# Optimization experiments

Hardware: AMD Instinct MI355X
Metric: run time of the kernel (lower is better)

The kernel has to match this reference:

```python
import jax, jax.numpy as jnp
import numpy as np
import math

N, J = 8192, 22  # N = batch*frames (per-frame calls are independent), J = num_joint


def _layernorm(x, g, b, eps=1e-5):
    m = jnp.mean(x, axis=-1, keepdims=True)
    v = jnp.var(x, axis=-1, keepdims=True)
    return (x - m) * jax.lax.rsqrt(v + eps) * g + b


def _attention(x, Wqkv, bqkv, Wo, bo, heads):
    # x: [B, n, d]; matches torch Attention (scale = d**-0.5)
    B, n, d = x.shape
    hd = d // heads
    qkv = (x @ Wqkv + bqkv).reshape(B, n, 3, heads, hd).transpose(2, 0, 3, 1, 4)
    q, k, v = qkv[0], qkv[1], qkv[2]  # [B, h, n, hd]
    dots = jnp.einsum('bhid,bhjd->bhij', q, k) * (d ** -0.5)
    attn = jax.nn.softmax(dots, axis=-1)
    out = jnp.einsum('bhij,bhjd->bhid', attn, v)
    out = out.transpose(0, 2, 1, 3).reshape(B, n, -1)
    return out @ Wo + bo


def _encoder(x, tok_W, tok_b, qkv_W, qkv_b, o_W, o_b, ln_g, ln_b, m1_W, m1_b, m2_W, m2_b, heads):
    tok = x @ tok_W + tok_b                                   # [B, J, 64]
    h = _attention(tok, qkv_W, qkv_b, o_W, o_b, heads)        # [B, J, out_dim]
    hn = _layernorm(h, ln_g, ln_b)
    mlp = jax.nn.relu(hn @ m1_W + m1_b) @ m2_W + m2_b
    return h + mlp                                            # Residual(LN+MLP)


def _sinusoidal_pe(max_len, dim):
    pos = np.arange(max_len)[:, None].astype(np.float32)
    div = np.exp(np.arange(0, dim, 2, dtype=np.float32) * (-math.log(10000.0) / dim))
    pe = np.zeros((max_len, dim), dtype=np.float32)
    pe[:, 0::2] = np.sin(pos * div)
    pe[:, 1::2] = np.cos(pos * div)
    return jnp.asarray(pe)


def setup_inputs() -> dict:
    key = jax.random.key(0)
    ks = iter(jax.random.split(key, 64))
    rn = lambda shape, s=0.1: jax.random.normal(next(ks), shape, dtype=jnp.float32) * s
    inp = {
        'q_t': jax.random.normal(next(ks), (N, J, 4), dtype=jnp.float32),
        'skelA': jax.random.normal(next(ks), (N, J, 3), dtype=jnp.float32),
        'skelB': jax.random.normal(next(ks), (N, J, 3), dtype=jnp.float32),
        'quat_mean': jax.random.normal(next(ks), (J, 4), dtype=jnp.float32) * 0.1,
        'quat_std': jax.random.uniform(next(ks), (J, 4), dtype=jnp.float32, minval=0.5, maxval=1.5),
        # QuatEncoder params
        'qe_tok_W': rn((4, 64)), 'qe_tok_b': jnp.zeros((64,), jnp.float32),
        'qe_qkv_W': rn((64, 192)), 'qe_qkv_b': jnp.zeros((192,), jnp.float32),
        'qe_o_W': rn((64, 256)), 'qe_o_b': jnp.zeros((256,), jnp.float32),
        'qe_ln_g': jnp.ones((256,), jnp.float32), 'qe_ln_b': jnp.zeros((256,), jnp.float32),
        'qe_m1_W': rn((256, 512)), 'qe_m1_b': jnp.zeros((512,), jnp.float32),
        'qe_m2_W': rn((512, 256)), 'qe_m2_b': jnp.zeros((256,), jnp.float32),
        # shared SeklEncoder params
        'se_tok_W': rn((3, 64)), 'se_tok_b': jnp.zeros((64,), jnp.float32),
        'se_qkv_W': rn((64, 192)), 'se_qkv_b': jnp.zeros((192,), jnp.float32),
        'se_o_W': rn((64, 128)), 'se_o_b': jnp.zeros((128,), jnp.float32),
        'se_ln_g': jnp.ones((128,), jnp.float32), 'se_ln_b': jnp.zeros((128,), jnp.float32),
        'se_m1_W': rn((128, 256)), 'se_m1_b': jnp.zeros((256,), jnp.float32),
        'se_m2_W': rn((256, 128)), 'se_m2_b': jnp.zeros((128,), jnp.float32),
        # head
        'emb_W': rn((512, 128)), 'emb_b': jnp.zeros((128,), jnp.float32),
        'del_W': rn((128, 4)), 'del_b': jnp.zeros((4,), jnp.float32),
    }
    return inp


def reference(q_t, skelA, skelB, quat_mean, quat_std,
              qe_tok_W, qe_tok_b, qe_qkv_W, qe_qkv_b, qe_o_W, qe_o_b,
              qe_ln_g, qe_ln_b, qe_m1_W, qe_m1_b, qe_m2_W, qe_m2_b,
              se_tok_W, se_tok_b, se_qkv_W, se_qkv_b, se_o_W, se_o_b,
              se_ln_g, se_ln_b, se_m1_W, se_m1_b, se_m2_W, se_m2_b,
              emb_W, emb_b, del_W, del_b):
    q_embed = _encoder(q_t, qe_tok_W, qe_tok_b, qe_qkv_W, qe_qkv_b, qe_o_W, qe_o_b,
                       qe_ln_g, qe_ln_b, qe_m1_W, qe_m1_b, qe_m2_W, qe_m2_b, heads=4)   # [N,J,256]
    sA = _encoder(skelA, se_tok_W, se_tok_b, se_qkv_W, se_qkv_b, se_o_W, se_o_b,
                  se_ln_g, se_ln_b, se_m1_W, se_m1_b, se_m2_W, se_m2_b, heads=2)        # [N,J,128]
    sB = _encoder(skelB, se_tok_W, se_tok_b, se_qkv_W, se_qkv_b, se_o_W, se_o_b,
                  se_ln_g, se_ln_b, se_m1_W, se_m1_b, se_m2_W, se_m2_b, heads=2)        # [N,J,128]
    cat = jnp.concatenate([q_embed, sA, sB], axis=-1)                                   # [N,J,512]
    dim = cat.shape[-1]
    pe = _sinusoidal_pe(J, dim)
    pos = cat * math.sqrt(dim) + pe[None, :, :]
    embed = jax.nn.relu(pos @ emb_W + emb_b)                                            # [N,J,128]
    delta = embed @ del_W + del_b                                                       # [N,J,4]
    delta = delta * quat_std + quat_mean
    # normalized()
    lengths = jnp.sqrt(jnp.sum(delta * delta, axis=-1, keepdims=True))
    return delta / lengths
```

## Files before the change

### kernel.cpp

```cpp
#include <hip/hip_runtime.h>
#include <hip/hip_bf16.h>
#include <math.h>

#define NJ 22
#define MROWS 44
#define PROWS 48
#define NRT 3

typedef float f4 __attribute__((ext_vector_type(4)));
typedef _Float16 h8 __attribute__((ext_vector_type(8)));

#define WOFF_QE_QKV 0
#define WOFF_QE_O   24576
#define WOFF_QE_M1  57344
#define WOFF_QE_M2  319488
#define WOFF_SE_QKV 581632
#define WOFF_SE_O   606208
#define WOFF_SE_M1  622592
#define WOFF_SE_M2  688128
#define WOFF_EMB    753664
#define W_TOTAL     884736

struct Smem {
    _Float16 XH[PROWS * 256];
    __align__(16) char U[PROWS * 128 * 4];
    float LNp[PROWS * 4], LNq[PROWS * 4];
    float Sx[MROWS * 4];
};

struct Args {
    const float *q_t, *skelA, *skelB;
    const float *qe_o_b, *qe_ln_g, *qe_ln_b, *qe_m1_b, *qe_m2_b;
    const float *se_o_b, *se_ln_g, *se_ln_b, *se_m1_b, *se_m2_b;
    const float *fqe, *fse;
    const _Float16 *W;
    _Float16 *cat;
};

__device__ __forceinline__ int swz(int r, int c) {
    return (((c >> 3) ^ (r & 7)) << 3) | (c & 7);
}

template<int NI, int KSTEPS, int LDA>
__device__ __forceinline__ void mfma_gemm(f4 (&acc)[NI][NRT],
        const _Float16 *AH,
        const _Float16 *BH, const _Float16 *BL,
        int wK, int koff, int w, int l) {
    const int m = l & 15, q = l >> 4;
#pragma unroll 1
    for (int s = 0; s < KSTEPS; s++) {
        const int ka = s * 32 + q * 8;
        h8 a[NRT];
#pragma unroll
        for (int rt = 0; rt < NRT; rt++) {
            int r = rt * 16 + m;
            a[rt] = *(const h8 *)(AH + r * LDA + (((ka >> 3) ^ (r & 7)) << 3));
        }
#pragma unroll
        for (int i = 0; i < NI; i++) {
            int n = (w + 4 * i) * 16 + m;
            int boff = n * wK + koff + ka;
            h8 bh = *(const h8 *)(BH + boff);
            h8 bl = *(const h8 *)(BL + boff);
#pragma unroll
            for (int rt = 0; rt < NRT; rt++) {
                acc[i][rt] = __builtin_amdgcn_mfma_f32_16x16x32_f16(a[rt], bh, acc[i][rt], 0, 0, 0);
                acc[i][rt] = __builtin_amdgcn_mfma_f32_16x16x32_f16(a[rt], bl, acc[i][rt], 0, 0, 0);
            }
        }
    }
}

template<int NH, int HD>
__device__ __forceinline__ void attention(Smem &sm, int t) {
    constexpr int SPL = HD / 16;
    if (t < NH * MROWS * SPL) {
        const int half = t & (SPL - 1);
        const int ur = t / SPL;
        const int hh = ur / MROWS;
        const int rr = ur - hh * MROWS;
        const int jb = (rr >= NJ) ? NJ : 0;
        const float *KF = (const float *)sm.U;
        const float *VF = KF + PROWS * 64;
        const int c0 = 64 + hh * HD + half * 16;
        float qv[16];
#pragma unroll
        for (int g = 0; g < 2; g++) {
            h8 qh = *(const h8 *)(sm.XH + rr * 256 + swz(rr, c0 + g * 8));
#pragma unroll
            for (int d = 0; d < 8; d++) qv[g * 8 + d] = (float)qh[d];
        }
        float s[NJ];
        float mx = -1e30f;
#pragma unroll
        for (int j = 0; j < NJ; j++) {
            const float *kp = KF + (jb + j) * 64 + hh * HD + half * 16;
            float acc = 0.f;
#pragma unroll
            for (int d = 0; d < 16; d += 4) {
                float4 v = *(const float4 *)(kp + d);
                acc += qv[d] * v.x + qv[d + 1] * v.y + qv[d + 2] * v.z + qv[d + 3] * v.w;
            }
            if constexpr (SPL == 2) acc += __shfl_xor(acc, 1);
            s[j] = acc * 0.125f;
            mx = fmaxf(mx, s[j]);
        }
        float sum = 0.f;
#pragma unroll
        for (int j = 0; j < NJ; j++) { s[j] = __expf(s[j] - mx); sum += s[j]; }
        float inv = 1.f / sum;
        float o[16];
#pragma unroll
        for (int d = 0; d < 16; d++) o[d] = 0.f;
#pragma unroll
        for (int j = 0; j < NJ; j++) {
            float p = s[j] * inv;
            const float *vp = VF + (jb + j) * 64 + hh * HD + half * 16;
#pragma unroll
            for (int d = 0; d < 16; d += 4) {
                float4 v = *(const float4 *)(vp + d);
                o[d] = fmaf(p, v.x, o[d]);       o[d + 1] = fmaf(p, v.y, o[d + 1]);
                o[d + 2] = fmaf(p, v.z, o[d + 2]); o[d + 3] = fmaf(p, v.w, o[d + 3]);
            }
        }
        const int cw = hh * HD + half * 16;
#pragma unroll
        for (int g = 0; g < 2; g++) {
            h8 oh;
#pragma unroll
            for (int d = 0; d < 8; d++) oh[d] = (_Float16)o[g * 8 + d];
            *(h8 *)(sm.XH + rr * 256 + swz(rr, cw + g * 8)) = oh;
        }
    }
}

template<int D, int NH, int TK>
__device__ __forceinline__ void encode(Smem &sm, const float *__restrict__ xg,
        const float *__restrict__ F,
        const float *__restrict__ oB,
        const float *__restrict__ lnG,  const float *__restrict__ lnB,
        const float *__restrict__ m1B,  const float *__restrict__ m2B,
        const _Float16 *__restrict__ Wo,
        const _Float16 *__restrict__ Wm1, const _Float16 *__restrict__ Wm2,
        _Float16 *__restrict__ catb, int catoff, int t, int w, int l) {
    constexpr int NI = D / 64;
    constexpr int HID = 2 * D;
    const int m = l & 15, q = l >> 4;
    const float *FW = F, *Fb = F + TK * 192;

    if (t < MROWS * TK) sm.Sx[t] = xg[t];
    __syncthreads();
    {
        float *KV = (float *)sm.U;
#pragma unroll
        for (int i = 0; i < 11; i++) {
            int r = w + 4 * i;
            float x0 = sm.Sx[r * TK + 0];
            float x1 = sm.Sx[r * TK + 1];
            float x2 = sm.Sx[r * TK + 2];
            float x3 = (TK == 4) ? sm.Sx[r * TK + 3] : 0.f;
#pragma unroll
            for (int kk = 0; kk < 3; kk++) {
                int c = kk * 64 + l;
                float acc = Fb[c];
                acc = fmaf(x0, FW[0 * 192 + c], acc);
                acc = fmaf(x1, FW[1 * 192 + c], acc);
                acc = fmaf(x2, FW[2 * 192 + c], acc);
                if (TK == 4) acc = fmaf(x3, FW[3 * 192 + c], acc);
                if (kk == 0)      sm.XH[r * 256 + swz(r, 64 + l)] = (_Float16)acc;
                else if (kk == 1) KV[r * 64 + l] = acc;
                else              KV[PROWS * 64 + r * 64 + l] = acc;
            }
        }
    }
    __syncthreads();
    attention<NH, 64 / NH>(sm, t);
    __syncthreads();
    f4 res[NI][NRT];
#pragma unroll
    for (int i = 0; i < NI; i++)
#pragma unroll
        for (int rt = 0; rt < NRT; rt++) res[i][rt] = (f4){0.f, 0.f, 0.f, 0.f};
    mfma_gemm<NI, 2, 256>(res, sm.XH, Wo, Wo + D * 64, 64, 0, w, l);
#pragma unroll
    for (int i = 0; i < NI; i++) {
        float b = oB[(w + 4 * i) * 16 + m];
#pragma unroll
        for (int rt = 0; rt < NRT; rt++)
#pragma unroll
            for (int e = 0; e < 4; e++) res[i][rt][e] += b;
    }
#pragma unroll
    for (int rt = 0; rt < NRT; rt++)
#pragma unroll
        for (int e = 0; e < 4; e++) {
            int r = rt * 16 + q * 4 + e;
            float s1 = 0.f, s2 = 0.f;
#pragma unroll
            for (int i = 0; i < NI; i++) {
                float v = res[i][rt][e];
                s1 += v; s2 = fmaf(v, v, s2);
            }
#pragma unroll
            for (int off = 8; off > 0; off >>= 1) {
                s1 += __shfl_xor(s1, off);
                s2 += __shfl_xor(s2, off);
            }
            if (m == 0) { sm.LNp[r * 4 + w] = s1; sm.LNq[r * 4 + w] = s2; }
        }
    __syncthreads();
    {
        float gv[NI], bv[NI];
#pragma unroll
        for (int i = 0; i < NI; i++) {
            int c = (w + 4 * i) * 16 + m;
            gv[i] = lnG[c]; bv[i] = lnB[c];
        }
#pragma unroll
        for (int rt = 0; rt < NRT; rt++)
#pragma unroll
            for (int e = 0; e < 4; e++) {
                int r = rt * 16 + q * 4 + e;
                float s1 = sm.LNp[r * 4] + sm.LNp[r * 4 + 1] + sm.LNp[r * 4 + 2] + sm.LNp[r * 4 + 3];
                float s2 = sm.LNq[r * 4] + sm.LNq[r * 4 + 1] + sm.LNq[r * 4 + 2] + sm.LNq[r * 4 + 3];
                float mean = s1 * (1.f / D);
                float var = s2 * (1.f / D) - mean * mean;
                float rinv = rsqrtf(fmaxf(var, 0.f) + 1e-5f);
#pragma unroll
                for (int i = 0; i < NI; i++) {
                    int c = (w + 4 * i) * 16 + m;
                    float v = (res[i][rt][e] - mean) * rinv * gv[i] + bv[i];
                    sm.XH[r * 256 + swz(r, c)] = (_Float16)v;
                }
            }
    }
    __syncthreads();
#pragma unroll 1
    for (int cb = 0; cb < HID / 128; cb++) {
        f4 h1[2][NRT];
#pragma unroll
        for (int i = 0; i < 2; i++)
#pragma unroll
            for (int rt = 0; rt < NRT; rt++) h1[i][rt] = (f4){0.f, 0.f, 0.f, 0.f};
        mfma_gemm<2, D / 32, 256>(h1, sm.XH,
                                  Wm1 + cb * 128 * D, Wm1 + HID * D + cb * 128 * D, D, 0, w, l);
        _Float16 *HH = (_Float16 *)sm.U + (cb & 1) * (PROWS * 128);
#pragma unroll
        for (int i = 0; i < 2; i++) {
            int c = (w + 4 * i) * 16 + m;
            float b = m1B[cb * 128 + c];
#pragma unroll
            for (int rt = 0; rt < NRT; rt++)
#pragma unroll
                for (int e = 0; e < 4; e++) {
                    int r = rt * 16 + q * 4 + e;
                    HH[r * 128 + swz(r, c)] = (_Float16)fmaxf(h1[i][rt][e] + b, 0.f);
                }
        }
        __syncthreads();
        mfma_gemm<NI, 4, 128>(res, HH, Wm2, Wm2 + D * HID, HID, cb * 128, w, l);
    }
#pragma unroll
    for (int i = 0; i < NI; i++) {
        int c = (w + 4 * i) * 16 + m;
        float b = m2B[c];
#pragma unroll
        for (int rt = 0; rt < NRT; rt++)
#pragma unroll
            for (int e = 0; e < 4; e++) {
                int r = rt * 16 + q * 4 + e;
                if (r < MROWS)
                    catb[r * 512 + catoff + c] = (_Float16)(res[i][rt][e] + b);
            }
    }
}

__global__ __launch_bounds__(256, 2) void fused_kernel(Args A) {
    __shared__ __align__(16) Smem sm;
    const int t = threadIdx.x, w = t >> 6, l = t & 63;
    const int blk = blockIdx.x;

    for (int i = t; i < 4 * 256; i += 256) {
        int r = MROWS + (i >> 8), c = i & 255;
        sm.XH[r * 256 + c] = (_Float16)0.f;
    }

    const _Float16 *W = A.W;
    _Float16 *catb = A.cat + (size_t)blk * MROWS * 512;

    encode<256, 4, 4>(sm, A.q_t + blk * MROWS * 4, A.fqe,
                      A.qe_o_b, A.qe_ln_g, A.qe_ln_b, A.qe_m1_b, A.qe_m2_b,
                      W + WOFF_QE_O, W + WOFF_QE_M1, W + WOFF_QE_M2,
                      catb, 0, t, w, l);
    encode<128, 2, 3>(sm, A.skelA + blk * MROWS * 3, A.fse,
                      A.se_o_b, A.se_ln_g, A.se_ln_b, A.se_m1_b, A.se_m2_b,
                      W + WOFF_SE_O, W + WOFF_SE_M1, W + WOFF_SE_M2,
                      catb, 256, t, w, l);
    encode<128, 2, 3>(sm, A.skelB + blk * MROWS * 3, A.fse,
                      A.se_o_b, A.se_ln_g, A.se_ln_b, A.se_m1_b, A.se_m2_b,
                      W + WOFF_SE_O, W + WOFF_SE_M1, W + WOFF_SE_M2,
                      catb, 384, t, w, l);
}

struct HeadArgs {
    const _Float16 *cat;
    const _Float16 *W;
    const float *P;
    const float *del_W, *del_b, *quat_mean, *quat_std;
    float *out;
    int R;
};

#define ELD 132

__global__ __launch_bounds__(256, 4) void head_kernel(HeadArgs A) {
    __shared__ float E[64 * ELD];
    __shared__ float Sd[64 * 4];
    const int t = threadIdx.x, w = t >> 6, l = t & 63;
    const int m = l & 15, q = l >> 4;
    const int rowbase = blockIdx.x * 64;
    const _Float16 *BH = A.W + WOFF_EMB;
    const _Float16 *BL = BH + 128 * 512;

    f4 acc[2][4];
#pragma unroll
    for (int i = 0; i < 2; i++)
#pragma unroll
        for (int rt = 0; rt < 4; rt++) acc[i][rt] = (f4){0.f, 0.f, 0.f, 0.f};

#pragma unroll 1
    for (int s = 0; s < 16; s++) {
        const int ka = s * 32 + q * 8;
        h8 a[4];
#pragma unroll
        for (int rt = 0; rt < 4; rt++) {
            int rg = rowbase + rt * 16 + m;
            rg = rg < A.R ? rg : A.R - 1;
            a[rt] = *(const h8 *)(A.cat + (size_t)rg * 512 + ka);
        }
#pragma unroll
        for (int i = 0; i < 2; i++) {
            int n = (w + 4 * i) * 16 + m;
            h8 bh = *(const h8 *)(BH + n * 512 + ka);
            h8 bl = *(const h8 *)(BL + n * 512 + ka);
#pragma unroll
            for (int rt = 0; rt < 4; rt++) {
                acc[i][rt] = __builtin_amdgcn_mfma_f32_16x16x32_f16(a[rt], bh, acc[i][rt], 0, 0, 0);
                acc[i][rt] = __builtin_amdgcn_mfma_f32_16x16x32_f16(a[rt], bl, acc[i][rt], 0, 0, 0);
            }
        }
    }
#pragma unroll
    for (int i = 0; i < 2; i++) {
        int c = (w + 4 * i) * 16 + m;
#pragma unroll
        for (int rt = 0; rt < 4; rt++)
#pragma unroll
            for (int e = 0; e < 4; e++) {
                int r = rt * 16 + q * 4 + e;
                int j = (rowbase + r) % NJ;
                float v = fmaf(22.627416997969522f, acc[i][rt][e], A.P[j * 128 + c]);
                E[r * ELD + c] = fmaxf(v, 0.f);
            }
    }
    __syncthreads();
    {
        int r = t >> 2, d = t & 3;
        float a2 = A.del_b[d];
        const float *Er = E + r * ELD;
#pragma unroll 4
        for (int c4 = 0; c4 < 32; c4++) {
            float4 ev = *(const float4 *)(Er + c4 * 4);
            a2 = fmaf(ev.x, A.del_W[(c4 * 4 + 0) * 4 + d], a2);
            a2 = fmaf(ev.y, A.del_W[(c4 * 4 + 1) * 4 + d], a2);
            a2 = fmaf(ev.z, A.del_W[(c4 * 4 + 2) * 4 + d], a2);
            a2 = fmaf(ev.w, A.del_W[(c4 * 4 + 3) * 4 + d], a2);
        }
        int j = (rowbase + r) % NJ;
        Sd[t] = fmaf(a2, A.quat_std[j * 4 + d], A.quat_mean[j * 4 + d]);
    }
    __syncthreads();
    {
        int r = t >> 2;
        int rg = rowbase + r;
        if (rg < A.R) {
            float x0 = Sd[r * 4], x1 = Sd[r * 4 + 1];
            float x2 = Sd[r * 4 + 2], x3 = Sd[r * 4 + 3];
            float inv = 1.f / sqrtf(x0 * x0 + x1 * x1 + x2 * x2 + x3 * x3);
            A.out[(size_t)rg * 4 + (t & 3)] = Sd[t] * inv;
        }
    }
}

struct WDesc { const float *W; int K; int N; int off; };
struct SplitArgs { WDesc d[9]; _Float16 *out; };

__global__ void split_kernel(SplitArgs a) {
    WDesc d = a.d[blockIdx.y];
    int e = blockIdx.x * 256 + threadIdx.x;
    int tot = d.K * d.N;
    if (e < tot) {
        int n = e / d.K, k = e - n * d.K;
        float v = d.W[k * d.N + n];
        _Float16 h = (_Float16)v;
        a.out[d.off + e] = h;
        a.out[d.off + tot + e] = (_Float16)(v - (float)h);
    }
}

struct FoldArgs {
    const float *qe_tokW, *qe_tokB, *qe_qkvW, *qe_qkvB;
    const float *se_tokW, *se_tokB, *se_qkvW, *se_qkvB;
    float *fqe, *fse;
};

__global__ void fold_kernel(FoldArgs a) {
    int c = threadIdx.x;
    if (blockIdx.x == 0) {
#pragma unroll
        for (int kk = 0; kk < 4; kk++) {
            float acc = 0.f;
            for (int k = 0; k < 64; k++)
                acc = fmaf(a.qe_tokW[kk * 64 + k], a.qe_qkvW[k * 192 + c], acc);
            a.fqe[kk * 192 + c] = acc;
        }
        float acc = a.qe_qkvB[c];
        for (int k = 0; k < 64; k++)
            acc = fmaf(a.qe_tokB[k], a.qe_qkvW[k * 192 + c], acc);
        a.fqe[4 * 192 + c] = acc;
    } else {
#pragma unroll
        for (int kk = 0; kk < 3; kk++) {
            float acc = 0.f;
            for (int k = 0; k < 64; k++)
                acc = fmaf(a.se_tokW[kk * 64 + k], a.se_qkvW[k * 192 + c], acc);
            a.fse[kk * 192 + c] = acc;
        }
        float acc = a.se_qkvB[c];
        for (int k = 0; k < 64; k++)
            acc = fmaf(a.se_tokB[k], a.se_qkvW[k * 192 + c], acc);
        a.fse[3 * 192 + c] = acc;
    }
}

__global__ void pe_emb_kernel(const float *__restrict__ emb_W,
                              const float *__restrict__ emb_b, float *P) {
    int r = blockIdx.x;
    int c = threadIdx.x;
    float acc = emb_b[c];
    const float k = -2.f * logf(10000.f) / 512.f;
    for (int i = 0; i < 256; i++) {
        float ang = (float)r * expf((float)i * k);
        acc = fmaf(sinf(ang), emb_W[(2 * i) * 128 + c], acc);
        acc = fmaf(cosf(ang), emb_W[(2 * i + 1) * 128 + c], acc);
    }
    P[r * 128 + c] = acc;
}

extern "C" void kernel_launch(void *const *d_in, const int *in_sizes, int n_in,
                              void *d_out, int out_size, void *d_ws, size_t ws_size,
                              hipStream_t stream) {
    const float **in = (const float **)d_in;
    float *dwf = (float *)d_ws;
    float *P   = dwf;
    float *FQE = dwf + 2816;
    float *FSE = dwf + 3776;
    _Float16 *W = (_Float16 *)(dwf + 4544);
    _Float16 *cat = W + W_TOTAL;

    Args A;
    A.q_t = in[0]; A.skelA = in[1]; A.skelB = in[2];
    A.qe_o_b = in[10]; A.qe_ln_g = in[11]; A.qe_ln_b = in[12];
    A.qe_m1_b = in[14]; A.qe_m2_b = in[16];
    A.se_o_b = in[22]; A.se_ln_g = in[23]; A.se_ln_b = in[24];
    A.se_m1_b = in[26]; A.se_m2_b = in[28];
    A.fqe = FQE; A.fse = FSE;
    A.W = W; A.cat = cat;

    SplitArgs sa;
    sa.d[0] = { in[7],  64, 192, WOFF_QE_QKV };
    sa.d[1] = { in[9],  64, 256, WOFF_QE_O };
    sa.d[2] = { in[13], 256, 512, WOFF_QE_M1 };
    sa.d[3] = { in[15], 512, 256, WOFF_QE_M2 };
    sa.d[4] = { in[19], 64, 192, WOFF_SE_QKV };
    sa.d[5] = { in[21], 64, 128, WOFF_SE_O };
    sa.d[6] = { in[25], 128, 256, WOFF_SE_M1 };
    sa.d[7] = { in[27], 256, 128, WOFF_SE_M2 };
    sa.d[8] = { in[29], 512, 128, WOFF_EMB };
    sa.out = W;

    FoldArgs fa;
    fa.qe_tokW = in[5];  fa.qe_tokB = in[6];  fa.qe_qkvW = in[7];  fa.qe_qkvB = in[8];
    fa.se_tokW = in[17]; fa.se_tokB = in[18]; fa.se_qkvW = in[19]; fa.se_qkvB = in[20];
    fa.fqe = FQE; fa.fse = FSE;

    int n_items = in_sizes[0] / (NJ * 4);
    int blocks = n_items / 2;
    int R = n_items * NJ;

    HeadArgs H;
    H.cat = cat; H.W = W; H.P = P;
    H.del_W = in[31]; H.del_b = in[32]; H.quat_mean = in[3]; H.quat_std = in[4];
    H.out = (float *)d_out; H.R = R;

    split_kernel<<<dim3(512, 9), 256, 0, stream>>>(sa);
    fold_kernel<<<2, 192, 0, stream>>>(fa);
    pe_emb_kernel<<<NJ, 128, 0, stream>>>(in[29], in[30], P);
    fused_kernel<<<blocks, 256, 0, stream>>>(A);
    head_kernel<<<(R + 63) / 64, 256, 0, stream>>>(H);
}
```

Before: 1.307 ms.

## Fuse embedding head into encoder kernel, keeping concatenated features in LDS

The head GEMM, ReLU, delta projection and normalization now run inside the fused encoder kernel. The encoder outputs stay in shared memory (the skeleton ones in new LDS buffers, the quaternion one in XH), so the fp16 concatenated tensor is no longer written to and re-read from global memory and one launch is dropped. Encoder order is swapped so the larger output lands last in XH. In exchange, LDS use per block grows, which may pressure occupancy. Each block also reloads the embedding weights and runs the GEMM on padded 48-row tiles.

```diff
diff --git a/kernel.cpp b/kernel.cpp
--- a/kernel.cpp
+++ b/kernel.cpp
@@ -24,6 +24,7 @@
 struct Smem {
     _Float16 XH[PROWS * 256];
     __align__(16) char U[PROWS * 128 * 4];
+    _Float16 PK[2][PROWS * 128];
     float LNp[PROWS * 4], LNq[PROWS * 4];
     float Sx[MROWS * 4];
 };
@@ -33,8 +34,10 @@
     const float *qe_o_b, *qe_ln_g, *qe_ln_b, *qe_m1_b, *qe_m2_b;
     const float *se_o_b, *se_ln_g, *se_ln_b, *se_m1_b, *se_m2_b;
     const float *fqe, *fse;
+    const float *P;
+    const float *del_W, *del_b, *quat_mean, *quat_std;
     const _Float16 *W;
-    _Float16 *cat;
+    float *out;
 };
 
 __device__ __forceinline__ int swz(int r, int c) {
@@ -142,7 +145,7 @@
         const float *__restrict__ m1B,  const float *__restrict__ m2B,
         const _Float16 *__restrict__ Wo,
         const _Float16 *__restrict__ Wm1, const _Float16 *__restrict__ Wm2,
-        _Float16 *__restrict__ catb, int catoff, int t, int w, int l) {
+        _Float16 *__restrict__ outp, int outLDA, int t, int w, int l) {
     constexpr int NI = D / 64;
     constexpr int HID = 2 * D;
     const int m = l & 15, q = l >> 4;
@@ -269,8 +272,7 @@
 #pragma unroll
             for (int e = 0; e < 4; e++) {
                 int r = rt * 16 + q * 4 + e;
-                if (r < MROWS)
-                    catb[r * 512 + catoff + c] = (_Float16)(res[i][rt][e] + b);
+                outp[r * outLDA + swz(r, c)] = (_Float16)(res[i][rt][e] + b);
             }
     }
 }
@@ -278,6 +280,7 @@
 __global__ __launch_bounds__(256, 2) void fused_kernel(Args A) {
     __shared__ __align__(16) Smem sm;
     const int t = threadIdx.x, w = t >> 6, l = t & 63;
+    const int m = l & 15, q = l >> 4;
     const int blk = blockIdx.x;
 
     for (int i = t; i < 4 * 256; i += 256) {
@@ -286,88 +289,53 @@
     }
 
     const _Float16 *W = A.W;
-    _Float16 *catb = A.cat + (size_t)blk * MROWS * 512;
-
+
+    encode<128, 2, 3>(sm, A.skelA + blk * MROWS * 3, A.fse,
+                      A.se_o_b, A.se_ln_g, A.se_ln_b, A.se_m1_b, A.se_m2_b,
+                      W + WOFF_SE_O, W + WOFF_SE_M1, W + WOFF_SE_M2,
+                      sm.PK[0], 128, t, w, l);
+    encode<128, 2, 3>(sm, A.skelB + blk * MROWS * 3, A.fse,
+                      A.se_o_b, A.se_ln_g, A.se_ln_b, A.se_m1_b, A.se_m2_b,
+                      W + WOFF_SE_O, W + WOFF_SE_M1, W + WOFF_SE_M2,
+                      sm.PK[1], 128, t, w, l);
     encode<256, 4, 4>(sm, A.q_t + blk * MROWS * 4, A.fqe,
                       A.qe_o_b, A.qe_ln_g, A.qe_ln_b, A.qe_m1_b, A.qe_m2_b,
                       W + WOFF_QE_O, W + WOFF_QE_M1, W + WOFF_QE_M2,
-                      catb, 0, t, w, l);
-    encode<128, 2, 3>(sm, A.skelA + blk * MROWS * 3, A.fse,
-                      A.se_o_b, A.se_ln_g, A.se_ln_b, A.se_m1_b, A.se_m2_b,
-                      W + WOFF_SE_O, W + WOFF_SE_M1, W + WOFF_SE_M2,
-                      catb, 256, t, w, l);
-    encode<128, 2, 3>(sm, A.skelB + blk * MROWS * 3, A.fse,
-                      A.se_o_b, A.se_ln_g, A.se_ln_b, A.se_m1_b, A.se_m2_b,
-                      W + WOFF_SE_O, W + WOFF_SE_M1, W + WOFF_SE_M2,
-                      catb, 384, t, w, l);
-}
-
-struct HeadArgs {
-    const _Float16 *cat;
-    const _Float16 *W;
-    const float *P;
-    const float *del_W, *del_b, *quat_mean, *quat_std;
-    float *out;
-    int R;
-};
-
-#define ELD 132
-
-__global__ __launch_bounds__(256, 4) void head_kernel(HeadArgs A) {
-    __shared__ float E[64 * ELD];
-    __shared__ float Sd[64 * 4];
-    const int t = threadIdx.x, w = t >> 6, l = t & 63;
-    const int m = l & 15, q = l >> 4;
-    const int rowbase = blockIdx.x * 64;
-    const _Float16 *BH = A.W + WOFF_EMB;
-    const _Float16 *BL = BH + 128 * 512;
-
-    f4 acc[2][4];
+                      sm.XH, 256, t, w, l);
+
+    __syncthreads();
+    const _Float16 *We = W + WOFF_EMB;
+    const _Float16 *WeL = We + 128 * 512;
+    f4 emb[2][NRT];
 #pragma unroll
     for (int i = 0; i < 2; i++)
 #pragma unroll
-        for (int rt = 0; rt < 4; rt++) acc[i][rt] = (f4){0.f, 0.f, 0.f, 0.f};
-
-#pragma unroll 1
-    for (int s = 0; s < 16; s++) {
-        const int ka = s * 32 + q * 8;
-        h8 a[4];
-#pragma unroll
-        for (int rt = 0; rt < 4; rt++) {
-            int rg = rowbase + rt * 16 + m;
-            rg = rg < A.R ? rg : A.R - 1;
-            a[rt] = *(const h8 *)(A.cat + (size_t)rg * 512 + ka);
-        }
-#pragma unroll
-        for (int i = 0; i < 2; i++) {
-            int n = (w + 4 * i) * 16 + m;
-            h8 bh = *(const h8 *)(BH + n * 512 + ka);
-            h8 bl = *(const h8 *)(BL + n * 512 + ka);
-#pragma unroll
-            for (int rt = 0; rt < 4; rt++) {
-                acc[i][rt] = __builtin_amdgcn_mfma_f32_16x16x32_f16(a[rt], bh, acc[i][rt], 0, 0, 0);
-                acc[i][rt] = __builtin_amdgcn_mfma_f32_16x16x32_f16(a[rt], bl, acc[i][rt], 0, 0, 0);
-            }
-        }
-    }
+        for (int rt = 0; rt < NRT; rt++) emb[i][rt] = (f4){0.f, 0.f, 0.f, 0.f};
+    mfma_gemm<2, 8, 256>(emb, sm.XH,   We, WeL, 512, 0,   w, l);
+    mfma_gemm<2, 4, 128>(emb, sm.PK[0], We, WeL, 512, 256, w, l);
+    mfma_gemm<2, 4, 128>(emb, sm.PK[1], We, WeL, 512, 384, w, l);
+    float *E = (float *)sm.U;
 #pragma unroll
     for (int i = 0; i < 2; i++) {
         int c = (w + 4 * i) * 16 + m;
 #pragma unroll
-        for (int rt = 0; rt < 4; rt++)
+        for (int rt = 0; rt < NRT; rt++)
 #pragma unroll
             for (int e = 0; e < 4; e++) {
                 int r = rt * 16 + q * 4 + e;
-                int j = (rowbase + r) % NJ;
-                float v = fmaf(22.627416997969522f, acc[i][rt][e], A.P[j * 128 + c]);
-                E[r * ELD + c] = fmaxf(v, 0.f);
-            }
-    }
-    __syncthreads();
-    {
+                if (r < MROWS) {
+                    int j = (r >= NJ) ? r - NJ : r;
+                    float v = fmaf(22.627416997969522f, emb[i][rt][e], A.P[j * 128 + c]);
+                    E[r * 132 + c] = fmaxf(v, 0.f);
+                }
+            }
+    }
+    __syncthreads();
+    float *Sd = sm.LNp;
+    if (t < MROWS * 4) {
         int r = t >> 2, d = t & 3;
         float a2 = A.del_b[d];
-        const float *Er = E + r * ELD;
+        const float *Er = E + r * 132;
 #pragma unroll 4
         for (int c4 = 0; c4 < 32; c4++) {
             float4 ev = *(const float4 *)(Er + c4 * 4);
@@ -376,19 +344,16 @@
             a2 = fmaf(ev.z, A.del_W[(c4 * 4 + 2) * 4 + d], a2);
             a2 = fmaf(ev.w, A.del_W[(c4 * 4 + 3) * 4 + d], a2);
         }
-        int j = (rowbase + r) % NJ;
+        int j = (r >= NJ) ? r - NJ : r;
         Sd[t] = fmaf(a2, A.quat_std[j * 4 + d], A.quat_mean[j * 4 + d]);
     }
     __syncthreads();
-    {
+    if (t < MROWS * 4) {
         int r = t >> 2;
-        int rg = rowbase + r;
-        if (rg < A.R) {
-            float x0 = Sd[r * 4], x1 = Sd[r * 4 + 1];
-            float x2 = Sd[r * 4 + 2], x3 = Sd[r * 4 + 3];
-            float inv = 1.f / sqrtf(x0 * x0 + x1 * x1 + x2 * x2 + x3 * x3);
-            A.out[(size_t)rg * 4 + (t & 3)] = Sd[t] * inv;
-        }
+        float x0 = Sd[r * 4], x1 = Sd[r * 4 + 1];
+        float x2 = Sd[r * 4 + 2], x3 = Sd[r * 4 + 3];
+        float inv = 1.f / sqrtf(x0 * x0 + x1 * x1 + x2 * x2 + x3 * x3);
+        A.out[((size_t)blk * MROWS + r) * 4 + (t & 3)] = Sd[t] * inv;
     }
 }
 
@@ -466,7 +431,6 @@
     float *FQE = dwf + 2816;
     float *FSE = dwf + 3776;
     _Float16 *W = (_Float16 *)(dwf + 4544);
-    _Float16 *cat = W + W_TOTAL;
 
     Args A;
     A.q_t = in[0]; A.skelA = in[1]; A.skelB = in[2];
@@ -475,7 +439,10 @@
     A.se_o_b = in[22]; A.se_ln_g = in[23]; A.se_ln_b = in[24];
     A.se_m1_b = in[26]; A.se_m2_b = in[28];
     A.fqe = FQE; A.fse = FSE;
-    A.W = W; A.cat = cat;
+    A.P = P;
+    A.del_W = in[31]; A.del_b = in[32];
+    A.quat_mean = in[3]; A.quat_std = in[4];
+    A.W = W; A.out = (float *)d_out;
 
     SplitArgs sa;
     sa.d[0] = { in[7],  64, 192, WOFF_QE_QKV };
@@ -496,16 +463,9 @@
 
     int n_items = in_sizes[0] / (NJ * 4);
     int blocks = n_items / 2;
-    int R = n_items * NJ;
-
-    HeadArgs H;
-    H.cat = cat; H.W = W; H.P = P;
-    H.del_W = in[31]; H.del_b = in[32]; H.quat_mean = in[3]; H.quat_std = in[4];
-    H.out = (float *)d_out; H.R = R;
 
     split_kernel<<<dim3(512, 9), 256, 0, stream>>>(sa);
     fold_kernel<<<2, 192, 0, stream>>>(fa);
     pe_emb_kernel<<<NJ, 128, 0, stream>>>(in[29], in[30], P);
     fused_kernel<<<blocks, 256, 0, stream>>>(A);
-    head_kernel<<<(R + 63) / 64, 256, 0, stream>>>(H);
-}
+}
```

Measured after the change: 1.286 ms. About the same (-1.6%).
